# Kernel tuning notes

Measured on AMD Instinct MI355X. Metric: run time of the kernel, lower is better.

Reference implementation:

```python
import jax, jax.numpy as jnp
import numpy as np

N = 131072
K = 1024
D = 64

def setup_inputs() -> dict:
    key = jax.random.key(0)
    k1, k2 = jax.random.split(key)
    x = jax.random.normal(k1, (N, D), dtype=jnp.float32)
    emb_weight = jax.random.normal(k2, (K, D), dtype=jnp.float32)
    return {"x": x, "emb_weight": emb_weight}

def reference(x, emb_weight):
    distances = (
        jnp.sum(x * x, axis=1, keepdims=True)
        + jnp.sum(emb_weight * emb_weight, axis=1)
        - 2.0 * jnp.matmul(x, emb_weight.T)
    )
    codebook_indices = jnp.argmin(distances, axis=1)  # [N]
    probs = jax.nn.one_hot(codebook_indices, K, dtype=x.dtype)  # [N, K]
    z_q = emb_weight[codebook_indices]  # [N, D]
    return (z_q, probs)
```

## Files before the change

kernel.cpp:

```cpp
#include <hip/hip_runtime.h>
#include <math.h>

#define N_TOK 131072
#define K_CB  1024
#define D_DIM 64
#define MARGIN 0.03f

#define WS_EN     0
#define WS_ES     4096
#define WS_CNT    266240
#define WS_LIST   266256

typedef short bf16x8 __attribute__((ext_vector_type(8)));
typedef float f32x4  __attribute__((ext_vector_type(4)));

__device__ __forceinline__ ushort f2bf(float f) {
    uint u = __float_as_uint(f);
    u += 0x7FFFu + ((u >> 16) & 1u);
    return (ushort)(u >> 16);
}
__device__ __forceinline__ float bf2f(ushort h) {
    return __uint_as_float(((uint)h) << 16);
}

__global__ __launch_bounds__(256) void prep_kernel(
    const float* __restrict__ emb, float* __restrict__ en,
    ushort* __restrict__ es, uint* __restrict__ fixcnt)
{
    const int tid = threadIdx.x;
    const int pb  = blockIdx.x;
    const int c6  = tid & 63;
    const int q   = tid >> 6;
    const int code = pb * 64 + c6;
    if (pb == 0 && tid == 0) *fixcnt = 0;

    const int cb = code >> 4, jj = code & 15;
    const float* er = emb + (size_t)code * D_DIM;
    #pragma unroll
    for (int j = 0; j < 16; ++j) {
        int d = q * 16 + j;
        float f = er[d];
        ushort h = f2bf(f);
        ushort l = f2bf(f - bf2f(h));
        int ks = d >> 5, quad = (d >> 3) & 3, e = d & 7;
        es[(size_t)(((cb * 4 + ks)     * 4 + quad) * 16 + jj) * 8 + e] = h;
        es[(size_t)(((cb * 4 + ks + 2) * 4 + quad) * 16 + jj) * 8 + e] = l;
    }
    if (q == 0) {
        float s = 0.f;
        #pragma unroll
        for (int d = 0; d < D_DIM; ++d) s = fmaf(er[d], er[d], s);
        en[code] = s;
    }
}

__global__ __launch_bounds__(256) void vq_onehot(
    const float* __restrict__ x, const float* __restrict__ emb,
    const float* __restrict__ en, const ushort* __restrict__ es,
    float* __restrict__ zq, float* __restrict__ probs,
    uint* __restrict__ fixcnt, uint* __restrict__ fixlist, uint fixcap)
{
    const int tid  = threadIdx.x;
    const int wave = tid >> 6, lane = tid & 63;
    const int quad = lane >> 4, l15 = lane & 15;
    const int rg = wave >> 1;
    const int h  = wave & 1;
    const int blockRow = blockIdx.x * 64;
    const int waveRowBase = blockRow + rg * 32;

    __shared__ float lds_b1[2][64];
    __shared__ float lds_b2[2][64];
    __shared__ int   lds_k1[2][64];
    __shared__ int   lds_bk[64];

    bf16x8 af[2][4];
    #pragma unroll
    for (int g = 0; g < 2; ++g) {
        const float* xr = x + (size_t)(waveRowBase + g * 16 + l15) * D_DIM + quad * 8;
        f32x4 p0 = *(const f32x4*)(xr);
        f32x4 p1 = *(const f32x4*)(xr + 4);
        f32x4 p2 = *(const f32x4*)(xr + 32);
        f32x4 p3 = *(const f32x4*)(xr + 36);
        float v0[8], v1[8];
        #pragma unroll
        for (int j = 0; j < 4; ++j) { v0[j] = p0[j]; v0[4 + j] = p1[j]; v1[j] = p2[j]; v1[4 + j] = p3[j]; }
        #pragma unroll
        for (int j = 0; j < 8; ++j) {
            ushort h0 = f2bf(v0[j]);
            af[g][0][j] = (short)h0;
            af[g][2][j] = (short)f2bf(v0[j] - bf2f(h0));
            ushort h1 = f2bf(v1[j]);
            af[g][1][j] = (short)h1;
            af[g][3][j] = (short)f2bf(v1[j] - bf2f(h1));
        }
    }

    float b1[8], b2[8]; int k1[8];
    #pragma unroll
    for (int s = 0; s < 8; ++s) { b1[s] = INFINITY; b2[s] = INFINITY; k1[s] = 0; }

    const bf16x8* __restrict__ esv = (const bf16x8*)es;
    const int fidx = quad * 16 + l15;
    const int cb0  = h * 32;

    bf16x8 bc[4]; float enc;
    #pragma unroll
    for (int ks = 0; ks < 4; ++ks) bc[ks] = esv[(size_t)cb0 * 256 + ks * 64 + fidx];
    enc = en[cb0 * 16 + l15];

    #pragma unroll 2
    for (int i = 0; i < 32; ++i) {
        const int cb  = cb0 + i;
        const int nbi = cb0 + ((i + 1) & 31);
        bf16x8 bn[4]; float enn;
        #pragma unroll
        for (int ks = 0; ks < 4; ++ks) bn[ks] = esv[(size_t)nbi * 256 + ks * 64 + fidx];
        enn = en[nbi * 16 + l15];

        f32x4 acc0 = {0.f, 0.f, 0.f, 0.f};
        f32x4 acc1 = {0.f, 0.f, 0.f, 0.f};
        acc0 = __builtin_amdgcn_mfma_f32_16x16x32_bf16(af[0][0], bc[0], acc0, 0, 0, 0);
        acc0 = __builtin_amdgcn_mfma_f32_16x16x32_bf16(af[0][1], bc[1], acc0, 0, 0, 0);
        acc0 = __builtin_amdgcn_mfma_f32_16x16x32_bf16(af[0][0], bc[2], acc0, 0, 0, 0);
        acc0 = __builtin_amdgcn_mfma_f32_16x16x32_bf16(af[0][1], bc[3], acc0, 0, 0, 0);
        acc0 = __builtin_amdgcn_mfma_f32_16x16x32_bf16(af[0][2], bc[0], acc0, 0, 0, 0);
        acc0 = __builtin_amdgcn_mfma_f32_16x16x32_bf16(af[0][3], bc[1], acc0, 0, 0, 0);
        acc1 = __builtin_amdgcn_mfma_f32_16x16x32_bf16(af[1][0], bc[0], acc1, 0, 0, 0);
        acc1 = __builtin_amdgcn_mfma_f32_16x16x32_bf16(af[1][1], bc[1], acc1, 0, 0, 0);
        acc1 = __builtin_amdgcn_mfma_f32_16x16x32_bf16(af[1][0], bc[2], acc1, 0, 0, 0);
        acc1 = __builtin_amdgcn_mfma_f32_16x16x32_bf16(af[1][1], bc[3], acc1, 0, 0, 0);
        acc1 = __builtin_amdgcn_mfma_f32_16x16x32_bf16(af[1][2], bc[0], acc1, 0, 0, 0);
        acc1 = __builtin_amdgcn_mfma_f32_16x16x32_bf16(af[1][3], bc[1], acc1, 0, 0, 0);

        const int code = cb * 16 + l15;
        #pragma unroll
        for (int r = 0; r < 4; ++r) {
            {
                float d = fmaf(-2.f, acc0[r], enc);
                bool lt = d < b1[r];
                b2[r] = lt ? b1[r] : fminf(b2[r], d);
                k1[r] = lt ? code : k1[r];
                b1[r] = lt ? d : b1[r];
            }
            {
                int s = 4 + r;
                float d = fmaf(-2.f, acc1[r], enc);
                bool lt = d < b1[s];
                b2[s] = lt ? b1[s] : fminf(b2[s], d);
                k1[s] = lt ? code : k1[s];
                b1[s] = lt ? d : b1[s];
            }
        }

        #pragma unroll
        for (int ks = 0; ks < 4; ++ks) bc[ks] = bn[ks];
        enc = enn;
    }

    #pragma unroll
    for (int s = 0; s < 8; ++s) {
        #pragma unroll
        for (int off = 1; off < 16; off <<= 1) {
            float ob1 = __shfl_xor(b1[s], off);
            int   ok1 = __shfl_xor(k1[s], off);
            float ob2 = __shfl_xor(b2[s], off);
            bool better = (ob1 < b1[s]) || (ob1 == b1[s] && ok1 < k1[s]);
            float loser = better ? b1[s] : ob1;
            b1[s] = better ? ob1 : b1[s];
            k1[s] = better ? ok1 : k1[s];
            b2[s] = fminf(fminf(b2[s], ob2), loser);
        }
    }

    if (l15 == 0) {
        #pragma unroll
        for (int s = 0; s < 8; ++s) {
            int idx = rg * 32 + (s >> 2) * 16 + quad * 4 + (s & 3);
            lds_b1[h][idx] = b1[s];
            lds_b2[h][idx] = b2[s];
            lds_k1[h][idx] = k1[s];
        }
    }
    __syncthreads();

    if (tid < 64) {
        float a1 = lds_b1[0][tid], a2 = lds_b2[0][tid]; int ak = lds_k1[0][tid];
        float c1 = lds_b1[1][tid], c2 = lds_b2[1][tid]; int ck = lds_k1[1][tid];
        bool bwin = c1 < a1;
        float m1 = bwin ? c1 : a1;
        int   mk = bwin ? ck : ak;
        float loser = bwin ? a1 : c1;
        float m2 = fminf(fminf(a2, c2), loser);
        lds_bk[tid] = mk;
        if (m2 - m1 <= MARGIN) {
            uint idx = atomicAdd(fixcnt, 1u);
            if (idx < fixcap) fixlist[idx] = (uint)(blockRow + tid) | ((uint)mk << 17);
        }
    }
    __syncthreads();

    #pragma unroll
    for (int mb = 0; mb < 4; ++mb) {
        int rl = wave * 16 + mb * 4 + quad;
        int bk = lds_bk[rl];
        f32x4 v = ((const f32x4*)(emb + (size_t)bk * D_DIM))[l15];
        ((f32x4*)(zq + (size_t)(blockRow + rl) * D_DIM))[l15] = v;
    }

    for (int m = 0; m < 16; ++m) {
        int rl = wave * 16 + m;
        int bk = lds_bk[rl];
        float* prow = probs + (size_t)(blockRow + rl) * K_CB;
        #pragma unroll
        for (int s = 0; s < 4; ++s) {
            int c = s * 256 + lane * 4;
            f32x4 v;
            v[0] = (c     == bk) ? 1.f : 0.f;
            v[1] = (c + 1 == bk) ? 1.f : 0.f;
            v[2] = (c + 2 == bk) ? 1.f : 0.f;
            v[3] = (c + 3 == bk) ? 1.f : 0.f;
            *(f32x4*)(prow + c) = v;
        }
    }
}

__global__ __launch_bounds__(256) void vq_fixup(
    const float* __restrict__ x, const float* __restrict__ emb,
    const float* __restrict__ en,
    float* __restrict__ zq, float* __restrict__ probs,
    const uint* __restrict__ fixcnt, const uint* __restrict__ fixlist, uint fixcap)
{
    const int lane = threadIdx.x & 63;
    const int quad = lane >> 4, l15 = lane & 15;
    const uint gwave = (uint)((blockIdx.x * 256 + threadIdx.x) >> 6);
    uint cnt = *fixcnt;
    if (cnt > fixcap) cnt = fixcap;

    for (uint e = gwave; e < cnt; e += 1024u) {
        uint w = fixlist[e];
        int row = (int)(w & 0x1FFFFu);
        int kg  = (int)(w >> 17);

        const f32x4* xr4 = (const f32x4*)(x + (size_t)row * D_DIM) + quad * 4;
        f32x4 xv[4];
        #pragma unroll
        for (int c = 0; c < 4; ++c) xv[c] = xr4[c];
        float xn = 0.f;
        #pragma unroll
        for (int c = 0; c < 4; ++c)
            #pragma unroll
            for (int j = 0; j < 4; ++j) xn = fmaf(xv[c][j], xv[c][j], xn);
        xn += __shfl_xor(xn, 16);
        xn += __shfl_xor(xn, 32);

        float bd = INFINITY; int bk = 0;
        for (int t = 0; t < 64; ++t) {
            int code = t * 16 + l15;
            const f32x4* er4 = (const f32x4*)(emb + (size_t)code * D_DIM) + quad * 4;
            float dot = 0.f;
            #pragma unroll
            for (int c = 0; c < 4; ++c) {
                f32x4 ev = er4[c];
                #pragma unroll
                for (int j = 0; j < 4; ++j) dot = fmaf(xv[c][j], ev[j], dot);
            }
            dot += __shfl_xor(dot, 16);
            dot += __shfl_xor(dot, 32);
            float dist = fmaf(-2.f, dot, xn + en[code]);
            if (dist < bd) { bd = dist; bk = code; }
        }
        #pragma unroll
        for (int off = 1; off < 16; off <<= 1) {
            float od = __shfl_xor(bd, off);
            int   ok = __shfl_xor(bk, off);
            if (od < bd || (od == bd && ok < bk)) { bd = od; bk = ok; }
        }
        if (bk != kg) {
            if (lane == 0) {
                probs[(size_t)row * K_CB + kg] = 0.f;
                probs[(size_t)row * K_CB + bk] = 1.f;
            }
            if (lane < 16)
                ((f32x4*)(zq + (size_t)row * D_DIM))[lane] =
                    ((const f32x4*)(emb + (size_t)bk * D_DIM))[lane];
        }
    }
}

extern "C" void kernel_launch(void* const* d_in, const int* in_sizes, int n_in,
                              void* d_out, int out_size, void* d_ws, size_t ws_size,
                              hipStream_t stream) {
    const float* x   = (const float*)d_in[0];
    const float* emb = (const float*)d_in[1];
    float* zq    = (float*)d_out;
    float* probs = (float*)d_out + (size_t)N_TOK * D_DIM;

    char* ws = (char*)d_ws;
    float*  en      = (float*)(ws + WS_EN);
    ushort* es      = (ushort*)(ws + WS_ES);
    uint*   fixcnt  = (uint*)(ws + WS_CNT);
    uint*   fixlist = (uint*)(ws + WS_LIST);
    uint fixcap = (ws_size > WS_LIST + 4) ? (uint)((ws_size - WS_LIST) / 4) : 0u;

    prep_kernel<<<16, 256, 0, stream>>>(emb, en, es, fixcnt);
    vq_onehot<<<N_TOK / 64, 256, 0, stream>>>(x, emb, en, es, zq, probs, fixcnt, fixlist, fixcap);
    vq_fixup<<<256, 256, 0, stream>>>(x, emb, en, zq, probs, fixcnt, fixlist, fixcap);
}
```

Baseline: 630.7 us.

## Move probs zero-fill into prep kernel and scatter one-hot ones

```diff
diff --git a/kernel.cpp b/kernel.cpp
--- a/kernel.cpp
+++ b/kernel.cpp
@@ -23,16 +23,27 @@
     return __uint_as_float(((uint)h) << 16);
 }
 
-__global__ __launch_bounds__(256) void prep_kernel(
+__global__ __launch_bounds__(256) void prep_fill(
     const float* __restrict__ emb, float* __restrict__ en,
-    ushort* __restrict__ es, uint* __restrict__ fixcnt)
+    ushort* __restrict__ es, uint* __restrict__ fixcnt,
+    float* __restrict__ probs)
 {
     const int tid = threadIdx.x;
-    const int pb  = blockIdx.x;
-    const int c6  = tid & 63;
-    const int q   = tid >> 6;
-    const int code = pb * 64 + c6;
-    if (pb == 0 && tid == 0) *fixcnt = 0;
+    const int b   = blockIdx.x;
+
+    {
+        const f32x4 z = {0.f, 0.f, 0.f, 0.f};
+        f32x4* p = (f32x4*)probs + (size_t)b * 16384 + tid;
+        #pragma unroll
+        for (int i = 0; i < 64; ++i) p[(size_t)i * 256] = z;
+    }
+
+    if (b >= 16) return;
+
+    const int c6   = tid & 63;
+    const int q    = tid >> 6;
+    const int code = b * 64 + c6;
+    if (b == 0 && tid == 0) *fixcnt = 0;
 
     const int cb = code >> 4, jj = code & 15;
     const float* er = emb + (size_t)code * D_DIM;
@@ -192,6 +203,7 @@
         float loser = bwin ? a1 : c1;
         float m2 = fminf(fminf(a2, c2), loser);
         lds_bk[tid] = mk;
+        probs[(size_t)(blockRow + tid) * K_CB + mk] = 1.0f;
         if (m2 - m1 <= MARGIN) {
             uint idx = atomicAdd(fixcnt, 1u);
             if (idx < fixcap) fixlist[idx] = (uint)(blockRow + tid) | ((uint)mk << 17);
@@ -205,22 +217,6 @@
         int bk = lds_bk[rl];
         f32x4 v = ((const f32x4*)(emb + (size_t)bk * D_DIM))[l15];
         ((f32x4*)(zq + (size_t)(blockRow + rl) * D_DIM))[l15] = v;
-    }
-
-    for (int m = 0; m < 16; ++m) {
-        int rl = wave * 16 + m;
-        int bk = lds_bk[rl];
-        float* prow = probs + (size_t)(blockRow + rl) * K_CB;
-        #pragma unroll
-        for (int s = 0; s < 4; ++s) {
-            int c = s * 256 + lane * 4;
-            f32x4 v;
-            v[0] = (c     == bk) ? 1.f : 0.f;
-            v[1] = (c + 1 == bk) ? 1.f : 0.f;
-            v[2] = (c + 2 == bk) ? 1.f : 0.f;
-            v[3] = (c + 3 == bk) ? 1.f : 0.f;
-            *(f32x4*)(prow + c) = v;
-        }
     }
 }
 
@@ -302,7 +298,7 @@
     uint*   fixlist = (uint*)(ws + WS_LIST);
     uint fixcap = (ws_size > WS_LIST + 4) ? (uint)((ws_size - WS_LIST) / 4) : 0u;
 
-    prep_kernel<<<16, 256, 0, stream>>>(emb, en, es, fixcnt);
+    prep_fill<<<2048, 256, 0, stream>>>(emb, en, es, fixcnt, probs);
     vq_onehot<<<N_TOK / 64, 256, 0, stream>>>(x, emb, en, es, zq, probs, fixcnt, fixlist, fixcap);
     vq_fixup<<<256, 256, 0, stream>>>(x, emb, en, zq, probs, fixcnt, fixlist, fixcap);
 }
```

New measurement: 676.8 us. +7.3%, slower.

## Pack distance and index into uint keys, interleave zero-fill probs stores with MFMA loop

Applied to the files above, without the earlier changes.

```diff
diff --git a/kernel.cpp b/kernel.cpp
--- a/kernel.cpp
+++ b/kernel.cpp
@@ -4,7 +4,7 @@
 #define N_TOK 131072
 #define K_CB  1024
 #define D_DIM 64
-#define MARGIN 0.03f
+#define MARGIN_U 72u
 
 #define WS_EN     0
 #define WS_ES     4096
@@ -68,10 +68,9 @@
     const int blockRow = blockIdx.x * 64;
     const int waveRowBase = blockRow + rg * 32;
 
-    __shared__ float lds_b1[2][64];
-    __shared__ float lds_b2[2][64];
-    __shared__ int   lds_k1[2][64];
-    __shared__ int   lds_bk[64];
+    __shared__ uint lds_b1[2][64];
+    __shared__ uint lds_b2[2][64];
+    __shared__ int  lds_bk[64];
 
     bf16x8 af[2][4];
     #pragma unroll
@@ -95,9 +94,9 @@
         }
     }
 
-    float b1[8], b2[8]; int k1[8];
-    #pragma unroll
-    for (int s = 0; s < 8; ++s) { b1[s] = INFINITY; b2[s] = INFINITY; k1[s] = 0; }
+    uint b1u[8], b2u[8];
+    #pragma unroll
+    for (int s = 0; s < 8; ++s) { b1u[s] = 0xFFFFFFFFu; b2u[s] = 0xFFFFFFFFu; }
 
     const bf16x8* __restrict__ esv = (const bf16x8*)es;
     const int fidx = quad * 16 + l15;
@@ -106,7 +105,10 @@
     bf16x8 bc[4]; float enc;
     #pragma unroll
     for (int ks = 0; ks < 4; ++ks) bc[ks] = esv[(size_t)cb0 * 256 + ks * 64 + fidx];
-    enc = en[cb0 * 16 + l15];
+    enc = fmaf(en[cb0 * 16 + l15], 2048.f, 1048576.f);
+
+    const f32x4 zv = {0.f, 0.f, 0.f, 0.f};
+    f32x4* pz0 = (f32x4*)probs + (size_t)blockRow * 256 + (size_t)wave * 128 + lane * 2;
 
     #pragma unroll 2
     for (int i = 0; i < 32; ++i) {
@@ -115,7 +117,13 @@
         bf16x8 bn[4]; float enn;
         #pragma unroll
         for (int ks = 0; ks < 4; ++ks) bn[ks] = esv[(size_t)nbi * 256 + ks * 64 + fidx];
-        enn = en[nbi * 16 + l15];
+        enn = fmaf(en[nbi * 16 + l15], 2048.f, 1048576.f);
+
+        {
+            f32x4* pz = pz0 + (size_t)i * 512;
+            __builtin_nontemporal_store(zv, pz);
+            __builtin_nontemporal_store(zv, pz + 1);
+        }
 
         f32x4 acc0 = {0.f, 0.f, 0.f, 0.f};
         f32x4 acc1 = {0.f, 0.f, 0.f, 0.f};
@@ -132,23 +140,21 @@
         acc1 = __builtin_amdgcn_mfma_f32_16x16x32_bf16(af[1][2], bc[0], acc1, 0, 0, 0);
         acc1 = __builtin_amdgcn_mfma_f32_16x16x32_bf16(af[1][3], bc[1], acc1, 0, 0, 0);
 
-        const int code = cb * 16 + l15;
+        const uint code = (uint)(cb * 16 + l15);
         #pragma unroll
         for (int r = 0; r < 4; ++r) {
             {
-                float d = fmaf(-2.f, acc0[r], enc);
-                bool lt = d < b1[r];
-                b2[r] = lt ? b1[r] : fminf(b2[r], d);
-                k1[r] = lt ? code : k1[r];
-                b1[r] = lt ? d : b1[r];
+                float f = fmaf(-4096.f, acc0[r], enc);
+                uint u = ((uint)f << 10) | code;
+                uint lo = min(b1u[r], u), hi = max(b1u[r], u);
+                b1u[r] = lo; b2u[r] = min(b2u[r], hi);
             }
             {
                 int s = 4 + r;
-                float d = fmaf(-2.f, acc1[r], enc);
-                bool lt = d < b1[s];
-                b2[s] = lt ? b1[s] : fminf(b2[s], d);
-                k1[s] = lt ? code : k1[s];
-                b1[s] = lt ? d : b1[s];
+                float f = fmaf(-4096.f, acc1[r], enc);
+                uint u = ((uint)f << 10) | code;
+                uint lo = min(b1u[s], u), hi = max(b1u[s], u);
+                b1u[s] = lo; b2u[s] = min(b2u[s], hi);
             }
         }
 
@@ -161,14 +167,11 @@
     for (int s = 0; s < 8; ++s) {
         #pragma unroll
         for (int off = 1; off < 16; off <<= 1) {
-            float ob1 = __shfl_xor(b1[s], off);
-            int   ok1 = __shfl_xor(k1[s], off);
-            float ob2 = __shfl_xor(b2[s], off);
-            bool better = (ob1 < b1[s]) || (ob1 == b1[s] && ok1 < k1[s]);
-            float loser = better ? b1[s] : ob1;
-            b1[s] = better ? ob1 : b1[s];
-            k1[s] = better ? ok1 : k1[s];
-            b2[s] = fminf(fminf(b2[s], ob2), loser);
+            uint o1 = (uint)__shfl_xor((int)b1u[s], off);
+            uint o2 = (uint)__shfl_xor((int)b2u[s], off);
+            uint lo = min(b1u[s], o1), hi = max(b1u[s], o1);
+            b1u[s] = lo;
+            b2u[s] = min(min(b2u[s], o2), hi);
         }
     }
 
@@ -176,23 +179,21 @@
         #pragma unroll
         for (int s = 0; s < 8; ++s) {
             int idx = rg * 32 + (s >> 2) * 16 + quad * 4 + (s & 3);
-            lds_b1[h][idx] = b1[s];
-            lds_b2[h][idx] = b2[s];
-            lds_k1[h][idx] = k1[s];
+            lds_b1[h][idx] = b1u[s];
+            lds_b2[h][idx] = b2u[s];
         }
     }
     __syncthreads();
 
     if (tid < 64) {
-        float a1 = lds_b1[0][tid], a2 = lds_b2[0][tid]; int ak = lds_k1[0][tid];
-        float c1 = lds_b1[1][tid], c2 = lds_b2[1][tid]; int ck = lds_k1[1][tid];
-        bool bwin = c1 < a1;
-        float m1 = bwin ? c1 : a1;
-        int   mk = bwin ? ck : ak;
-        float loser = bwin ? a1 : c1;
-        float m2 = fminf(fminf(a2, c2), loser);
+        uint a1 = lds_b1[0][tid], a2 = lds_b2[0][tid];
+        uint c1 = lds_b1[1][tid], c2 = lds_b2[1][tid];
+        uint m1 = min(a1, c1);
+        uint m2 = min(min(a2, c2), max(a1, c1));
+        int  mk = (int)(m1 & 1023u);
         lds_bk[tid] = mk;
-        if (m2 - m1 <= MARGIN) {
+        probs[(size_t)(blockRow + tid) * K_CB + mk] = 1.0f;
+        if ((m2 >> 10) - (m1 >> 10) <= MARGIN_U) {
             uint idx = atomicAdd(fixcnt, 1u);
             if (idx < fixcap) fixlist[idx] = (uint)(blockRow + tid) | ((uint)mk << 17);
         }
@@ -204,23 +205,7 @@
         int rl = wave * 16 + mb * 4 + quad;
         int bk = lds_bk[rl];
         f32x4 v = ((const f32x4*)(emb + (size_t)bk * D_DIM))[l15];
-        ((f32x4*)(zq + (size_t)(blockRow + rl) * D_DIM))[l15] = v;
-    }
-
-    for (int m = 0; m < 16; ++m) {
-        int rl = wave * 16 + m;
-        int bk = lds_bk[rl];
-        float* prow = probs + (size_t)(blockRow + rl) * K_CB;
-        #pragma unroll
-        for (int s = 0; s < 4; ++s) {
-            int c = s * 256 + lane * 4;
-            f32x4 v;
-            v[0] = (c     == bk) ? 1.f : 0.f;
-            v[1] = (c + 1 == bk) ? 1.f : 0.f;
-            v[2] = (c + 2 == bk) ? 1.f : 0.f;
-            v[3] = (c + 3 == bk) ? 1.f : 0.f;
-            *(f32x4*)(prow + c) = v;
-        }
+        __builtin_nontemporal_store(v, (f32x4*)(zq + (size_t)(blockRow + rl) * D_DIM) + l15);
     }
 }
 
@@ -236,7 +221,7 @@
     uint cnt = *fixcnt;
     if (cnt > fixcap) cnt = fixcap;
 
-    for (uint e = gwave; e < cnt; e += 1024u) {
+    for (uint e = gwave; e < cnt; e += 4096u) {
         uint w = fixlist[e];
         int row = (int)(w & 0x1FFFFu);
         int kg  = (int)(w >> 17);
@@ -254,6 +239,7 @@
         xn += __shfl_xor(xn, 32);
 
         float bd = INFINITY; int bk = 0;
+        #pragma unroll 2
         for (int t = 0; t < 64; ++t) {
             int code = t * 16 + l15;
             const f32x4* er4 = (const f32x4*)(emb + (size_t)code * D_DIM) + quad * 4;
@@ -304,5 +290,5 @@
 
     prep_kernel<<<16, 256, 0, stream>>>(emb, en, es, fixcnt);
     vq_onehot<<<N_TOK / 64, 256, 0, stream>>>(x, emb, en, es, zq, probs, fixcnt, fixlist, fixcap);
-    vq_fixup<<<256, 256, 0, stream>>>(x, emb, en, zq, probs, fixcnt, fixlist, fixcap);
-}
+    vq_fixup<<<1024, 256, 0, stream>>>(x, emb, en, zq, probs, fixcnt, fixlist, fixcap);
+}
```

Result: slower. 744.7 us (+18.1%).
